# Performance work log

Hardware: AMD Instinct MI355X
Metric: run time of the kernel (lower is better)

## Reference

```python
import jax, jax.numpy as jnp
import numpy as np

D_MODEL = 1024
D_STATE = 16
D_CONV = 4
EXPAND = 2
D_INNER = EXPAND * D_MODEL  # 2048
BATCH = 2
SEQ = 2048


def setup_inputs() -> dict:
    key = jax.random.key(0)
    ks = jax.random.split(key, 7)
    s = 0.02
    x = jax.random.normal(ks[0], (BATCH, SEQ, D_MODEL), jnp.float32)
    in_proj_w = jax.random.normal(ks[1], (2 * D_INNER, D_MODEL), jnp.float32) * s
    conv_w = jax.random.normal(ks[2], (D_INNER, 1, D_CONV), jnp.float32) * s  # depthwise: groups=d_inner
    conv_b = jnp.zeros((D_INNER,), jnp.float32)
    x_proj_w = jax.random.normal(ks[3], (2 * D_STATE, D_INNER), jnp.float32) * s
    dt_proj_w = jax.random.normal(ks[4], (D_INNER, D_INNER), jnp.float32) * s
    dt_proj_b = jnp.zeros((D_INNER,), jnp.float32)
    # A = arange(1..d_state) repeated for each inner channel; A_log = log(A)
    A_log = jnp.log(jnp.tile(jnp.arange(1, D_STATE + 1, dtype=jnp.float32), (D_INNER, 1)))
    D_param = jnp.ones((D_INNER,), jnp.float32)
    out_proj_w = jax.random.normal(ks[5], (D_MODEL, D_INNER), jnp.float32) * s
    return {"x": x, "in_proj_w": in_proj_w, "conv_w": conv_w, "conv_b": conv_b,
            "x_proj_w": x_proj_w, "dt_proj_w": dt_proj_w, "dt_proj_b": dt_proj_b,
            "A_log": A_log, "D_param": D_param, "out_proj_w": out_proj_w}


def reference(x, in_proj_w, conv_w, conv_b, x_proj_w, dt_proj_w, dt_proj_b, A_log, D_param, out_proj_w):
    B, L, _ = x.shape
    # input projection -> [B, L, 2*d_inner], split into ssm path and gate
    xz = x @ in_proj_w.T
    x_ssm, z = jnp.split(xz, 2, axis=-1)

    # causal depthwise conv1d (torch pads both sides by d_conv-1 then slices [:L])
    xc = jnp.transpose(x_ssm, (0, 2, 1))  # [B, d_inner, L]
    xc = jnp.pad(xc, ((0, 0), (0, 0), (D_CONV - 1, 0)))
    xc = jax.lax.conv_general_dilated(
        xc, conv_w, window_strides=(1,), padding='VALID',
        dimension_numbers=('NCH', 'OIH', 'NCH'), feature_group_count=D_INNER)
    xc = xc + conv_b[None, :, None]
    x_act = jax.nn.silu(jnp.transpose(xc, (0, 2, 1)))  # [B, L, d_inner]

    delta = jax.nn.softplus(x_act @ dt_proj_w.T + dt_proj_b)  # [B, L, d_inner]
    bc = x_act @ x_proj_w.T                                   # [B, L, 2*d_state]
    B_p, C_p = jnp.split(bc, 2, axis=-1)

    A = -jnp.exp(A_log)  # [d_inner, d_state]

    def step(h, inp):
        u_i, d_i, B_i, C_i = inp  # [B,d], [B,d], [B,n], [B,n]
        dA = jnp.exp(d_i[..., None] * A)                       # [B, d, n]
        h = dA * h + (d_i * u_i)[..., None] * B_i[:, None, :]  # [B, d, n]
        y = jnp.einsum('bdn,bn->bd', h, C_i)
        return h, y

    h0 = jnp.zeros((B, D_INNER, D_STATE), x.dtype)
    seq = (jnp.swapaxes(x_act, 0, 1), jnp.swapaxes(delta, 0, 1),
           jnp.swapaxes(B_p, 0, 1), jnp.swapaxes(C_p, 0, 1))
    _, ys = jax.lax.scan(step, h0, seq)  # ys: [L, B, d_inner]
    y_ssm = jnp.swapaxes(ys, 0, 1) + x_act * D_param

    y = y_ssm * jax.nn.silu(z)
    return y @ out_proj_w.T
```

## Files before the change

kernel.cpp:

```cpp
#include <hip/hip_runtime.h>
#include <hip/hip_bf16.h>
#include <math.h>

#define DM 1024
#define DS 16
#define DI 2048
#define NB 2
#define LL 2048
#define BL (NB*LL)
#define LC 32
#define NC (LL/LC)

typedef __attribute__((ext_vector_type(8))) short short8;
typedef __attribute__((ext_vector_type(8))) unsigned short ushort8;
typedef __attribute__((ext_vector_type(4))) float f32x4;

__device__ __forceinline__ float silu_f(float x){ return x / (1.f + __expf(-x)); }
__device__ __forceinline__ float softplus_f(float x){ return (x > 15.f) ? x : log1pf(__expf(x)); }
__device__ __forceinline__ unsigned short f2bf(float f){
  unsigned u = __float_as_uint(f);
  u += 0x7fff + ((u >> 16) & 1);
  return (unsigned short)(u >> 16);
}
__device__ __forceinline__ float bf2f(unsigned short v){
  return __uint_as_float(((unsigned)v) << 16);
}

__global__ __launch_bounds__(256) void f2b_k(const float* __restrict__ src,
                                             unsigned short* __restrict__ dst, int n)
{
  int i = (blockIdx.x * 256 + threadIdx.x) * 8;
  if (i >= n) return;
  float4 v0 = *(const float4*)&src[i];
  float4 v1 = *(const float4*)&src[i + 4];
  ushort8 o;
  o[0]=f2bf(v0.x); o[1]=f2bf(v0.y); o[2]=f2bf(v0.z); o[3]=f2bf(v0.w);
  o[4]=f2bf(v1.x); o[5]=f2bf(v1.y); o[6]=f2bf(v1.z); o[7]=f2bf(v1.w);
  *(ushort8*)&dst[i] = o;
}

__global__ __launch_bounds__(256) void f2b_multi(
    const float* __restrict__ s0, unsigned short* __restrict__ d0, int c0,
    const float* __restrict__ s1, unsigned short* __restrict__ d1, int c1,
    const float* __restrict__ s2, unsigned short* __restrict__ d2, int c2,
    const float* __restrict__ s3, unsigned short* __restrict__ d3, int c3)
{
  int b = blockIdx.x;
  const float* s; unsigned short* d;
  if (b < c0)              { s = s0; d = d0; }
  else if ((b -= c0) < c1) { s = s1; d = d1; }
  else if ((b -= c1) < c2) { s = s2; d = d2; }
  else                     { b -= c2; s = s3; d = d3; }
  int i = (b * 256 + threadIdx.x) * 8;
  float4 v0 = *(const float4*)&s[i];
  float4 v1 = *(const float4*)&s[i + 4];
  ushort8 o;
  o[0]=f2bf(v0.x); o[1]=f2bf(v0.y); o[2]=f2bf(v0.z); o[3]=f2bf(v0.w);
  o[4]=f2bf(v1.x); o[5]=f2bf(v1.y); o[6]=f2bf(v1.z); o[7]=f2bf(v1.w);
  *(ushort8*)&d[i] = o;
}

template<int BN, int WAVESN, int EPI, int OUTBF>
__global__ __launch_bounds__(512, 2) void gemm3(
    const unsigned short* __restrict__ A, const unsigned short* __restrict__ Bw,
    const float* __restrict__ bias, void* __restrict__ Cp,
    int M, int N, int K)
{
  constexpr int BM = 256;
  constexpr int WM = BM / (8 / WAVESN);
  constexpr int WN = BN / WAVESN;
  constexpr int MR = WM / 16;
  constexpr int NRJ = WN / 16;
  constexpr int SLOADS = 4 + BN / 64;
  __shared__ unsigned short lds[2][(BM + BN) * 64];
  const int t = threadIdx.x;
  const int wid = t >> 6, lane = t & 63;
  const int nbx = N / BN;
  const int cpx = (nbx * (M / BM)) >> 3;
  const int bid = (int)blockIdx.x;
  const int swz = (bid & 7) * cpx + (bid >> 3);
  const int bm = (swz / nbx) * BM, bn = (swz % nbx) * BN;
  const int wm = (wid / WAVESN) * WM, wn = (wid % WAVESN) * WN;
  const int srow8 = lane >> 3;
  const int sch   = lane & 7;

  f32x4 acc[MR][NRJ] = {};

  auto stage = [&](int buf, int kt) {
    const int k0 = kt * 64;
    #pragma unroll
    for (int p = 0; p < 4; p++) {
      int row = p * 64 + wid * 8 + srow8;
      int ch = sch ^ (row & 7);
      __builtin_amdgcn_global_load_lds(
        (const __attribute__((address_space(1))) void*)(A + (size_t)(bm + row) * K + k0 + ch * 8),
        (__attribute__((address_space(3))) void*)(&lds[buf][(p * 64 + wid * 8) * 64]), 16, 0, 0);
    }
    #pragma unroll
    for (int p = 0; p < BN / 64; p++) {
      int row = p * 64 + wid * 8 + srow8;
      int ch = sch ^ (row & 7);
      __builtin_amdgcn_global_load_lds(
        (const __attribute__((address_space(1))) void*)(Bw + (size_t)(bn + row) * K + k0 + ch * 8),
        (__attribute__((address_space(3))) void*)(&lds[buf][(BM + p * 64 + wid * 8) * 64]), 16, 0, 0);
    }
  };

  const int nk = K / 64;
  stage(0, 0);
  stage(1, 1);
  asm volatile("s_waitcnt vmcnt(%0)" :: "n"(SLOADS) : "memory");
  __builtin_amdgcn_s_barrier();

  int cur = 0;
  for (int kt = 0; kt < nk; kt++) {
    const unsigned short* bufA = &lds[cur][0];
    const unsigned short* bufB = &lds[cur][BM * 64];
    #pragma unroll
    for (int ks = 0; ks < 2; ks++) {
      short8 af[MR], bfr[NRJ];
      #pragma unroll
      for (int i = 0; i < MR; i++) {
        int r = wm + i * 16 + (lane & 15);
        int c = ((ks << 2) + (lane >> 4)) ^ (r & 7);
        af[i] = *(const short8*)&bufA[r * 64 + c * 8];
      }
      #pragma unroll
      for (int j = 0; j < NRJ; j++) {
        int r = wn + j * 16 + (lane & 15);
        int c = ((ks << 2) + (lane >> 4)) ^ (r & 7);
        bfr[j] = *(const short8*)&bufB[r * 64 + c * 8];
      }
      #pragma unroll
      for (int i = 0; i < MR; i++)
        #pragma unroll
        for (int j = 0; j < NRJ; j++)
          acc[i][j] = __builtin_amdgcn_mfma_f32_16x16x32_bf16(af[i], bfr[j], acc[i][j], 0, 0, 0);
    }
    if (kt < nk - 2) {
      __builtin_amdgcn_s_barrier();
      stage(cur, kt + 2);
      asm volatile("s_waitcnt vmcnt(%0)" :: "n"(SLOADS) : "memory");
      __builtin_amdgcn_s_barrier();
    } else if (kt == nk - 2) {
      asm volatile("s_waitcnt vmcnt(0)" ::: "memory");
      __builtin_amdgcn_s_barrier();
    }
    cur ^= 1;
  }

  #pragma unroll
  for (int i = 0; i < MR; i++) {
    #pragma unroll
    for (int j = 0; j < NRJ; j++) {
      int col = bn + wn + j * 16 + (lane & 15);
      float bv = (EPI == 1) ? bias[col] : 0.f;
      #pragma unroll
      for (int r = 0; r < 4; r++) {
        int row = bm + wm + i * 16 + (lane >> 4) * 4 + r;
        float v = acc[i][j][r];
        if (EPI == 1) v = softplus_f(v + bv);
        if (OUTBF) ((unsigned short*)Cp)[(size_t)row * N + col] = f2bf(v);
        else       ((float*)Cp)[(size_t)row * N + col] = v;
      }
    }
  }
}

__global__ __launch_bounds__(256) void conv_silu_k(
    const unsigned short* __restrict__ xz, const float* __restrict__ cw,
    const float* __restrict__ cb, unsigned short* __restrict__ xa)
{
  int v = blockIdx.x * 256 + threadIdx.x;
  int d8 = (v & (DI/8 - 1)) * 8;
  int bl = v >> 8;
  int l  = bl & (LL - 1);
  float acc[8];
  #pragma unroll
  for (int j = 0; j < 8; j++) acc[j] = cb[d8 + j];
  size_t rowb = (size_t)bl * (2 * DI) + d8;
  #pragma unroll
  for (int k = 0; k < 4; k++) {
    int ls = l - 3 + k;
    if (ls >= 0) {
      ushort8 xv = *(const ushort8*)&xz[rowb + (size_t)(k - 3) * (2 * DI)];
      #pragma unroll
      for (int j = 0; j < 8; j++) acc[j] += bf2f(xv[j]) * cw[(d8 + j) * 4 + k];
    }
  }
  ushort8 o;
  #pragma unroll
  for (int j = 0; j < 8; j++) o[j] = f2bf(silu_f(acc[j]));
  *(ushort8*)&xa[(size_t)bl * DI + d8] = o;
}

__global__ __launch_bounds__(256) void bc_k(
    const unsigned short* __restrict__ xa, const unsigned short* __restrict__ w,
    float* __restrict__ bc)
{
  __shared__ unsigned short sx[8 * DI];
  const int t = threadIdx.x;
  const size_t base = (size_t)blockIdx.x * 8 * DI;
  #pragma unroll
  for (int it = 0; it < 8; it++) {
    int v = t + it * 256;
    *(ushort8*)&sx[v * 8] = *(const ushort8*)&xa[base + (size_t)v * 8];
  }
  __syncthreads();
  const int m = t >> 5, n = t & 31;
  const unsigned short* wr = w + (size_t)n * DI;
  const unsigned short* xr = sx + m * DI;
  float acc = 0.f;
  #pragma unroll 4
  for (int k = 0; k < DI; k += 8) {
    ushort8 xv = *(const ushort8*)&xr[k];
    ushort8 wv = *(const ushort8*)&wr[k];
    #pragma unroll
    for (int j = 0; j < 8; j++) acc += bf2f(xv[j]) * bf2f(wv[j]);
  }
  bc[(size_t)(blockIdx.x * 8 + m) * 32 + n] = acc;
}

__global__ __launch_bounds__(256) void scan_part1(
    const float* __restrict__ dlt, const unsigned short* __restrict__ xa,
    const float* __restrict__ bc, const float* __restrict__ A_log,
    float* __restrict__ S_arr, float* __restrict__ sumdlt)
{
  const int bid = blockIdx.x;
  const int b = bid >> 9;
  const int c = (bid >> 3) & (NC - 1);
  const int dg = bid & 7;
  const int t = threadIdx.x;
  const int d = dg * 256 + t;
  float Ac[16];
  #pragma unroll
  for (int n = 0; n < 16; n++) Ac[n] = -__expf(A_log[d * 16 + n]);
  __shared__ float sB[LC][16];
  for (int e = t; e < LC * 16; e += 256) {
    int l = e >> 4, n = e & 15;
    sB[l][n] = bc[(size_t)(b * LL + c * LC + l) * 32 + n];
  }
  __syncthreads();
  float h[16] = {};
  float sd = 0.f;
  size_t rowbase = (size_t)(b * LL + c * LC) * DI + d;
  for (int l = 0; l < LC; l++) {
    float dl = dlt[rowbase + (size_t)l * DI];
    float u  = bf2f(xa[rowbase + (size_t)l * DI]);
    float w = dl * u;
    sd += dl;
    #pragma unroll
    for (int n = 0; n < 16; n++) {
      float dA = __expf(dl * Ac[n]);
      h[n] = dA * h[n] + w * sB[l][n];
    }
  }
  float* Sp = S_arr + ((size_t)(b * NC + c) * DI + d) * 16;
  #pragma unroll
  for (int n = 0; n < 16; n++) Sp[n] = h[n];
  sumdlt[(size_t)(b * NC + c) * DI + d] = sd;
}

__global__ __launch_bounds__(256) void scan_combine(
    const float* __restrict__ A_log, const float* __restrict__ sumdlt,
    float* __restrict__ S_arr)
{
  int tid = blockIdx.x * 256 + threadIdx.x;
  int n = tid & 15;
  int d = (tid >> 4) & (DI - 1);
  int b = tid >> 15;
  float Ac = -__expf(A_log[d * 16 + n]);
  float h = 0.f;
  for (int c = 0; c < NC; c++) {
    size_t idx = ((size_t)(b * NC + c) * DI + d) * 16 + n;
    float S = S_arr[idx];
    float P = __expf(sumdlt[(size_t)(b * NC + c) * DI + d] * Ac);
    S_arr[idx] = h;
    h = P * h + S;
  }
}

__global__ __launch_bounds__(256) void scan_part2(
    const float* __restrict__ dlt, const unsigned short* __restrict__ xa,
    const float* __restrict__ bc, const float* __restrict__ A_log,
    const float* __restrict__ Dp, const unsigned short* __restrict__ xz,
    const float* __restrict__ Hin, unsigned short* __restrict__ y)
{
  const int bid = blockIdx.x;
  const int b = bid >> 9;
  const int c = (bid >> 3) & (NC - 1);
  const int dg = bid & 7;
  const int t = threadIdx.x;
  const int d = dg * 256 + t;
  float Ac[16];
  #pragma unroll
  for (int n = 0; n < 16; n++) Ac[n] = -__expf(A_log[d * 16 + n]);
  __shared__ float sB[LC][16];
  __shared__ float sC[LC][16];
  for (int e = t; e < LC * 16; e += 256) {
    int l = e >> 4, n = e & 15;
    size_t row = (size_t)(b * LL + c * LC + l) * 32;
    sB[l][n] = bc[row + n];
    sC[l][n] = bc[row + 16 + n];
  }
  __syncthreads();
  float h[16];
  const float* Hp = Hin + ((size_t)(b * NC + c) * DI + d) * 16;
  #pragma unroll
  for (int n = 0; n < 16; n++) h[n] = Hp[n];
  const float Dv = Dp[d];
  size_t rowbase = (size_t)(b * LL + c * LC) * DI + d;
  for (int l = 0; l < LC; l++) {
    float dl = dlt[rowbase + (size_t)l * DI];
    float u  = bf2f(xa[rowbase + (size_t)l * DI]);
    float w = dl * u;
    float ya = 0.f;
    #pragma unroll
    for (int n = 0; n < 16; n++) {
      float dA = __expf(dl * Ac[n]);
      h[n] = dA * h[n] + w * sB[l][n];
      ya += h[n] * sC[l][n];
    }
    float zz = bf2f(xz[(size_t)(b * LL + c * LC + l) * (2 * DI) + DI + d]);
    y[rowbase + (size_t)l * DI] = f2bf((ya + u * Dv) * silu_f(zz));
  }
}

extern "C" void kernel_launch(void* const* d_in, const int* in_sizes, int n_in,
                              void* d_out, int out_size, void* d_ws, size_t ws_size,
                              hipStream_t stream)
{
  const float* x    = (const float*)d_in[0];
  const float* Win  = (const float*)d_in[1];
  const float* cw   = (const float*)d_in[2];
  const float* cb   = (const float*)d_in[3];
  const float* Wxp  = (const float*)d_in[4];
  const float* Wdt  = (const float*)d_in[5];
  const float* bdt  = (const float*)d_in[6];
  const float* Alog = (const float*)d_in[7];
  const float* Dp   = (const float*)d_in[8];
  const float* Wout = (const float*)d_in[9];
  float* out = (float*)d_out;

  float* ws = (float*)d_ws;
  float* dlt    = ws;
  float* bcb    = dlt + 8388608;
  float* S_arr  = bcb + 131072;
  float* sumdlt = S_arr + 4194304;
  unsigned short* xz_bf = (unsigned short*)(sumdlt + 262144);
  unsigned short* xa_bf = xz_bf + 16777216;
  unsigned short* y_bf  = xa_bf + 8388608;
  unsigned short* x_bf  = y_bf;
  unsigned short* win_bf= y_bf + 4194304;
  unsigned short* wbuf  = y_bf + 8388608;
  unsigned short* wxp_bf= wbuf + 4194304;

  f2b_multi<<<dim3(2048 + 2048 + 2048 + 32), dim3(256), 0, stream>>>(
      x, x_bf, 2048, Win, win_bf, 2048, Wdt, wbuf, 2048, Wxp, wxp_bf, 32);
  gemm3<256,4,0,1><<<dim3(256), dim3(512), 0, stream>>>(x_bf, win_bf, nullptr, xz_bf, BL, 2*DI, DM);
  conv_silu_k<<<dim3(BL*DI/8/256), dim3(256), 0, stream>>>(xz_bf, cw, cb, xa_bf);
  gemm3<128,2,1,0><<<dim3(256), dim3(512), 0, stream>>>(xa_bf, wbuf, bdt, dlt, BL, DI, DI);
  f2b_k<<<dim3(DM*DI/2048), dim3(256), 0, stream>>>(Wout, wbuf, DM*DI);
  bc_k<<<dim3(BL/8), dim3(256), 0, stream>>>(xa_bf, wxp_bf, bcb);
  scan_part1<<<dim3(NB*NC*8), dim3(256), 0, stream>>>(dlt, xa_bf, bcb, Alog, S_arr, sumdlt);
  scan_combine<<<dim3(NB*DI*DS/256), dim3(256), 0, stream>>>(Alog, sumdlt, S_arr);
  scan_part2<<<dim3(NB*NC*8), dim3(256), 0, stream>>>(dlt, xa_bf, bcb, Alog, Dp, xz_bf, S_arr, y_bf);
  gemm3<64,2,0,0><<<dim3(256), dim3(512), 0, stream>>>(y_bf, wbuf, nullptr, out, BL, DM, DI);
}
```

Measured before the change: 346.5 us.

## Replace GEMM with triple-buffered, compile-time-K pipeline and retune tile shapes

Replaces the double-buffered GEMM with a triple-buffered version that prefetches three K-tiles ahead and fully unrolls the K loop using a compile-time K. Tile shapes change: all GEMMs use a 4x2 wave layout, and the in-projection uses 256x128 tiles over 512 blocks. The swizzle in the LDS fragment reads is simplified to lane-based XOR, which matches the store swizzle because row&7 equals lane&7 for these rows. Launch bounds drop to one block per CU, trading occupancy for deeper prefetch and more LDS.

```diff
diff --git a/kernel.cpp b/kernel.cpp
--- a/kernel.cpp
+++ b/kernel.cpp
@@ -60,27 +60,27 @@
   *(ushort8*)&d[i] = o;
 }
 
-template<int BN, int WAVESN, int EPI, int OUTBF>
-__global__ __launch_bounds__(512, 2) void gemm3(
+template<int BM, int BN, int KK, int EPI, int OUTBF>
+__global__ __launch_bounds__(512, 1) void gemm4(
     const unsigned short* __restrict__ A, const unsigned short* __restrict__ Bw,
     const float* __restrict__ bias, void* __restrict__ Cp,
-    int M, int N, int K)
-{
-  constexpr int BM = 256;
-  constexpr int WM = BM / (8 / WAVESN);
-  constexpr int WN = BN / WAVESN;
+    int M, int N)
+{
+  constexpr int WM = BM / 4;
+  constexpr int WN = BN / 2;
   constexpr int MR = WM / 16;
   constexpr int NRJ = WN / 16;
-  constexpr int SLOADS = 4 + BN / 64;
-  __shared__ unsigned short lds[2][(BM + BN) * 64];
+  constexpr int SL = (BM + BN) / 64;
+  constexpr int NK = KK / 64;
+  __shared__ unsigned short lds[3][(BM + BN) * 64];
   const int t = threadIdx.x;
   const int wid = t >> 6, lane = t & 63;
   const int nbx = N / BN;
-  const int cpx = (nbx * (M / BM)) >> 3;
+  const int cpx = (int)gridDim.x >> 3;
   const int bid = (int)blockIdx.x;
   const int swz = (bid & 7) * cpx + (bid >> 3);
   const int bm = (swz / nbx) * BM, bn = (swz % nbx) * BN;
-  const int wm = (wid / WAVESN) * WM, wn = (wid % WAVESN) * WN;
+  const int wm = (wid >> 1) * WM, wn = (wid & 1) * WN;
   const int srow8 = lane >> 3;
   const int sch   = lane & 7;
 
@@ -89,11 +89,11 @@
   auto stage = [&](int buf, int kt) {
     const int k0 = kt * 64;
     #pragma unroll
-    for (int p = 0; p < 4; p++) {
+    for (int p = 0; p < BM / 64; p++) {
       int row = p * 64 + wid * 8 + srow8;
       int ch = sch ^ (row & 7);
       __builtin_amdgcn_global_load_lds(
-        (const __attribute__((address_space(1))) void*)(A + (size_t)(bm + row) * K + k0 + ch * 8),
+        (const __attribute__((address_space(1))) void*)(A + (size_t)(bm + row) * KK + k0 + ch * 8),
         (__attribute__((address_space(3))) void*)(&lds[buf][(p * 64 + wid * 8) * 64]), 16, 0, 0);
     }
     #pragma unroll
@@ -101,34 +101,27 @@
       int row = p * 64 + wid * 8 + srow8;
       int ch = sch ^ (row & 7);
       __builtin_amdgcn_global_load_lds(
-        (const __attribute__((address_space(1))) void*)(Bw + (size_t)(bn + row) * K + k0 + ch * 8),
+        (const __attribute__((address_space(1))) void*)(Bw + (size_t)(bn + row) * KK + k0 + ch * 8),
         (__attribute__((address_space(3))) void*)(&lds[buf][(BM + p * 64 + wid * 8) * 64]), 16, 0, 0);
     }
   };
 
-  const int nk = K / 64;
-  stage(0, 0);
-  stage(1, 1);
-  asm volatile("s_waitcnt vmcnt(%0)" :: "n"(SLOADS) : "memory");
-  __builtin_amdgcn_s_barrier();
-
-  int cur = 0;
-  for (int kt = 0; kt < nk; kt++) {
-    const unsigned short* bufA = &lds[cur][0];
-    const unsigned short* bufB = &lds[cur][BM * 64];
+  auto compute = [&](int buf) {
+    const unsigned short* bufA = &lds[buf][0];
+    const unsigned short* bufB = &lds[buf][BM * 64];
     #pragma unroll
     for (int ks = 0; ks < 2; ks++) {
       short8 af[MR], bfr[NRJ];
       #pragma unroll
       for (int i = 0; i < MR; i++) {
         int r = wm + i * 16 + (lane & 15);
-        int c = ((ks << 2) + (lane >> 4)) ^ (r & 7);
+        int c = ((ks << 2) + (lane >> 4)) ^ (lane & 7);
         af[i] = *(const short8*)&bufA[r * 64 + c * 8];
       }
       #pragma unroll
       for (int j = 0; j < NRJ; j++) {
         int r = wn + j * 16 + (lane & 15);
-        int c = ((ks << 2) + (lane >> 4)) ^ (r & 7);
+        int c = ((ks << 2) + (lane >> 4)) ^ (lane & 7);
         bfr[j] = *(const short8*)&bufB[r * 64 + c * 8];
       }
       #pragma unroll
@@ -137,17 +130,27 @@
         for (int j = 0; j < NRJ; j++)
           acc[i][j] = __builtin_amdgcn_mfma_f32_16x16x32_bf16(af[i], bfr[j], acc[i][j], 0, 0, 0);
     }
-    if (kt < nk - 2) {
-      __builtin_amdgcn_s_barrier();
-      stage(cur, kt + 2);
-      asm volatile("s_waitcnt vmcnt(%0)" :: "n"(SLOADS) : "memory");
-      __builtin_amdgcn_s_barrier();
-    } else if (kt == nk - 2) {
-      asm volatile("s_waitcnt vmcnt(0)" ::: "memory");
-      __builtin_amdgcn_s_barrier();
-    }
-    cur ^= 1;
-  }
+  };
+
+  stage(0, 0); stage(1, 1); stage(2, 2);
+  asm volatile("s_waitcnt vmcnt(%0)" :: "n"(2 * SL) : "memory");
+  __builtin_amdgcn_s_barrier();
+
+  #pragma unroll
+  for (int kt = 0; kt <= NK - 4; kt++) {
+    compute(kt % 3);
+    __builtin_amdgcn_s_barrier();
+    stage(kt % 3, kt + 3);
+    asm volatile("s_waitcnt vmcnt(%0)" :: "n"(2 * SL) : "memory");
+    __builtin_amdgcn_s_barrier();
+  }
+  compute((NK - 3) % 3);
+  asm volatile("s_waitcnt vmcnt(%0)" :: "n"(SL) : "memory");
+  __builtin_amdgcn_s_barrier();
+  compute((NK - 2) % 3);
+  asm volatile("s_waitcnt vmcnt(0)" ::: "memory");
+  __builtin_amdgcn_s_barrier();
+  compute((NK - 1) % 3);
 
   #pragma unroll
   for (int i = 0; i < MR; i++) {
@@ -357,13 +360,13 @@
 
   f2b_multi<<<dim3(2048 + 2048 + 2048 + 32), dim3(256), 0, stream>>>(
       x, x_bf, 2048, Win, win_bf, 2048, Wdt, wbuf, 2048, Wxp, wxp_bf, 32);
-  gemm3<256,4,0,1><<<dim3(256), dim3(512), 0, stream>>>(x_bf, win_bf, nullptr, xz_bf, BL, 2*DI, DM);
+  gemm4<256,128,1024,0,1><<<dim3(512), dim3(512), 0, stream>>>(x_bf, win_bf, nullptr, xz_bf, BL, 2*DI);
   conv_silu_k<<<dim3(BL*DI/8/256), dim3(256), 0, stream>>>(xz_bf, cw, cb, xa_bf);
-  gemm3<128,2,1,0><<<dim3(256), dim3(512), 0, stream>>>(xa_bf, wbuf, bdt, dlt, BL, DI, DI);
+  gemm4<256,128,2048,1,0><<<dim3(256), dim3(512), 0, stream>>>(xa_bf, wbuf, bdt, dlt, BL, DI);
   f2b_k<<<dim3(DM*DI/2048), dim3(256), 0, stream>>>(Wout, wbuf, DM*DI);
   bc_k<<<dim3(BL/8), dim3(256), 0, stream>>>(xa_bf, wxp_bf, bcb);
   scan_part1<<<dim3(NB*NC*8), dim3(256), 0, stream>>>(dlt, xa_bf, bcb, Alog, S_arr, sumdlt);
   scan_combine<<<dim3(NB*DI*DS/256), dim3(256), 0, stream>>>(Alog, sumdlt, S_arr);
   scan_part2<<<dim3(NB*NC*8), dim3(256), 0, stream>>>(dlt, xa_bf, bcb, Alog, Dp, xz_bf, S_arr, y_bf);
-  gemm3<64,2,0,0><<<dim3(256), dim3(512), 0, stream>>>(y_bf, wbuf, nullptr, out, BL, DM, DI);
-}
+  gemm4<256,64,2048,0,0><<<dim3(256), dim3(512), 0, stream>>>(y_bf, wbuf, nullptr, out, BL, DM);
+}
```

After: 337.1 us. 1.03x faster.

## Replace templated GEMM with fixed 128x256 tile and overlapped load/MFMA schedule

Applied to the files above, without the earlier changes.

Replaces the gemm3 template, which used a 256-row tile and per-GEMM N widths, with gemm5, which uses a fixed 128x256 tile, 8 waves of 64x64, and launch bounds of one block per SIMD set. The main loop now reads all LDS fragments first, issues the next global->LDS stage, and then runs the MFMAs behind sched_barriers, so memory traffic overlaps compute. All three GEMMs use the new kernel with adjusted grid sizes. The output GEMM drops to 128 blocks, which risks underfilling the GPU, and the larger register footprint lowers occupancy.

```diff
diff --git a/kernel.cpp b/kernel.cpp
--- a/kernel.cpp
+++ b/kernel.cpp
@@ -60,99 +60,102 @@
   *(ushort8*)&d[i] = o;
 }
 
-template<int BN, int WAVESN, int EPI, int OUTBF>
-__global__ __launch_bounds__(512, 2) void gemm3(
+template<int EPI, int OUTBF>
+__global__ __launch_bounds__(512, 1) void gemm5(
     const unsigned short* __restrict__ A, const unsigned short* __restrict__ Bw,
     const float* __restrict__ bias, void* __restrict__ Cp,
-    int M, int N, int K)
-{
-  constexpr int BM = 256;
-  constexpr int WM = BM / (8 / WAVESN);
-  constexpr int WN = BN / WAVESN;
-  constexpr int MR = WM / 16;
-  constexpr int NRJ = WN / 16;
-  constexpr int SLOADS = 4 + BN / 64;
+    int N, int K)
+{
+  constexpr int BM = 128, BN = 256;
   __shared__ unsigned short lds[2][(BM + BN) * 64];
-  const int t = threadIdx.x;
-  const int wid = t >> 6, lane = t & 63;
+  const int t0 = threadIdx.x;
+  const int wid = t0 >> 6, lane = t0 & 63;
   const int nbx = N / BN;
-  const int cpx = (nbx * (M / BM)) >> 3;
+  const int cpx = (int)gridDim.x >> 3;
   const int bid = (int)blockIdx.x;
   const int swz = (bid & 7) * cpx + (bid >> 3);
   const int bm = (swz / nbx) * BM, bn = (swz % nbx) * BN;
-  const int wm = (wid / WAVESN) * WM, wn = (wid % WAVESN) * WN;
-  const int srow8 = lane >> 3;
-  const int sch   = lane & 7;
-
-  f32x4 acc[MR][NRJ] = {};
+  const int wm = (wid >> 2) * 64, wn = (wid & 3) * 64;
+
+  f32x4 acc[4][4] = {};
 
   auto stage = [&](int buf, int kt) {
     const int k0 = kt * 64;
     #pragma unroll
-    for (int p = 0; p < 4; p++) {
-      int row = p * 64 + wid * 8 + srow8;
-      int ch = sch ^ (row & 7);
+    for (int s = 0; s < 6; s++) {
+      int g = wid * 6 + s;
+      int row = g * 8 + (lane >> 3);
+      int ch  = (lane & 7) ^ (lane >> 3);
+      const unsigned short* src;
+      if (g < 16) src = A  + (size_t)(bm + row) * K + k0 + ch * 8;
+      else        src = Bw + (size_t)(bn + row - BM) * K + k0 + ch * 8;
       __builtin_amdgcn_global_load_lds(
-        (const __attribute__((address_space(1))) void*)(A + (size_t)(bm + row) * K + k0 + ch * 8),
-        (__attribute__((address_space(3))) void*)(&lds[buf][(p * 64 + wid * 8) * 64]), 16, 0, 0);
-    }
-    #pragma unroll
-    for (int p = 0; p < BN / 64; p++) {
-      int row = p * 64 + wid * 8 + srow8;
-      int ch = sch ^ (row & 7);
-      __builtin_amdgcn_global_load_lds(
-        (const __attribute__((address_space(1))) void*)(Bw + (size_t)(bn + row) * K + k0 + ch * 8),
-        (__attribute__((address_space(3))) void*)(&lds[buf][(BM + p * 64 + wid * 8) * 64]), 16, 0, 0);
+          (const __attribute__((address_space(1))) void*)src,
+          (__attribute__((address_space(3))) void*)(&lds[buf][(size_t)g * 512]), 16, 0, 0);
     }
   };
 
-  const int nk = K / 64;
   stage(0, 0);
   stage(1, 1);
-  asm volatile("s_waitcnt vmcnt(%0)" :: "n"(SLOADS) : "memory");
+  asm volatile("s_waitcnt vmcnt(6)" ::: "memory");
   __builtin_amdgcn_s_barrier();
 
-  int cur = 0;
-  for (int kt = 0; kt < nk; kt++) {
-    const unsigned short* bufA = &lds[cur][0];
-    const unsigned short* bufB = &lds[cur][BM * 64];
-    #pragma unroll
-    for (int ks = 0; ks < 2; ks++) {
-      short8 af[MR], bfr[NRJ];
-      #pragma unroll
-      for (int i = 0; i < MR; i++) {
-        int r = wm + i * 16 + (lane & 15);
-        int c = ((ks << 2) + (lane >> 4)) ^ (r & 7);
-        af[i] = *(const short8*)&bufA[r * 64 + c * 8];
-      }
-      #pragma unroll
-      for (int j = 0; j < NRJ; j++) {
-        int r = wn + j * 16 + (lane & 15);
-        int c = ((ks << 2) + (lane >> 4)) ^ (r & 7);
-        bfr[j] = *(const short8*)&bufB[r * 64 + c * 8];
-      }
-      #pragma unroll
-      for (int i = 0; i < MR; i++)
-        #pragma unroll
-        for (int j = 0; j < NRJ; j++)
-          acc[i][j] = __builtin_amdgcn_mfma_f32_16x16x32_bf16(af[i], bfr[j], acc[i][j], 0, 0, 0);
-    }
-    if (kt < nk - 2) {
-      __builtin_amdgcn_s_barrier();
-      stage(cur, kt + 2);
-      asm volatile("s_waitcnt vmcnt(%0)" :: "n"(SLOADS) : "memory");
-      __builtin_amdgcn_s_barrier();
-    } else if (kt == nk - 2) {
-      asm volatile("s_waitcnt vmcnt(0)" ::: "memory");
-      __builtin_amdgcn_s_barrier();
-    }
-    cur ^= 1;
-  }
-
-  #pragma unroll
-  for (int i = 0; i < MR; i++) {
-    #pragma unroll
-    for (int j = 0; j < NRJ; j++) {
+  const int nk = K >> 6;
+
+#define G5_READS(Q)                                                          \
+  short8 af[2][4], bfr[2][4];                                                \
+  _Pragma("unroll")                                                          \
+  for (int ks = 0; ks < 2; ks++) {                                           \
+    int cc = ((ks << 2) + (lane >> 4)) ^ (lane & 7);                         \
+    _Pragma("unroll")                                                        \
+    for (int i = 0; i < 4; i++) {                                            \
+      af[ks][i]  = *(const short8*)&lds[Q][(wm + i * 16 + (lane & 15)) * 64 + cc * 8]; \
+      bfr[ks][i] = *(const short8*)&lds[Q][BM * 64 + (wn + i * 16 + (lane & 15)) * 64 + cc * 8]; \
+    }                                                                        \
+  }
+
+#define G5_MFMA()                                                            \
+  _Pragma("unroll")                                                          \
+  for (int ks = 0; ks < 2; ks++)                                             \
+    _Pragma("unroll")                                                        \
+    for (int i = 0; i < 4; i++)                                              \
+      _Pragma("unroll")                                                      \
+      for (int j = 0; j < 4; j++)                                            \
+        acc[i][j] = __builtin_amdgcn_mfma_f32_16x16x32_bf16(af[ks][i], bfr[ks][j], acc[i][j], 0, 0, 0);
+
+  for (int t = 0; t < nk - 2; t++) {
+    const int q = t & 1;
+    G5_READS(q)
+    asm volatile("s_waitcnt lgkmcnt(0)" ::: "memory");
+    __builtin_amdgcn_sched_barrier(0);
+    __builtin_amdgcn_s_barrier();
+    stage(q, t + 2);
+    __builtin_amdgcn_sched_barrier(0);
+    G5_MFMA()
+    __builtin_amdgcn_sched_barrier(0);
+    asm volatile("s_waitcnt vmcnt(6)" ::: "memory");
+    __builtin_amdgcn_s_barrier();
+  }
+  {
+    const int q = (nk - 2) & 1;
+    G5_READS(q)
+    G5_MFMA()
+    __builtin_amdgcn_sched_barrier(0);
+    asm volatile("s_waitcnt vmcnt(0)" ::: "memory");
+    __builtin_amdgcn_s_barrier();
+  }
+  {
+    const int q = (nk - 1) & 1;
+    G5_READS(q)
+    G5_MFMA()
+  }
+#undef G5_READS
+#undef G5_MFMA
+
+  #pragma unroll
+  for (int i = 0; i < 4; i++) {
+    #pragma unroll
+    for (int j = 0; j < 4; j++) {
       int col = bn + wn + j * 16 + (lane & 15);
       float bv = (EPI == 1) ? bias[col] : 0.f;
       #pragma unroll
@@ -357,13 +360,13 @@
 
   f2b_multi<<<dim3(2048 + 2048 + 2048 + 32), dim3(256), 0, stream>>>(
       x, x_bf, 2048, Win, win_bf, 2048, Wdt, wbuf, 2048, Wxp, wxp_bf, 32);
-  gemm3<256,4,0,1><<<dim3(256), dim3(512), 0, stream>>>(x_bf, win_bf, nullptr, xz_bf, BL, 2*DI, DM);
+  gemm5<0,1><<<dim3(512), dim3(512), 0, stream>>>(x_bf, win_bf, nullptr, xz_bf, 2*DI, DM);
   conv_silu_k<<<dim3(BL*DI/8/256), dim3(256), 0, stream>>>(xz_bf, cw, cb, xa_bf);
-  gemm3<128,2,1,0><<<dim3(256), dim3(512), 0, stream>>>(xa_bf, wbuf, bdt, dlt, BL, DI, DI);
+  gemm5<1,0><<<dim3(256), dim3(512), 0, stream>>>(xa_bf, wbuf, bdt, dlt, DI, DI);
   f2b_k<<<dim3(DM*DI/2048), dim3(256), 0, stream>>>(Wout, wbuf, DM*DI);
   bc_k<<<dim3(BL/8), dim3(256), 0, stream>>>(xa_bf, wxp_bf, bcb);
   scan_part1<<<dim3(NB*NC*8), dim3(256), 0, stream>>>(dlt, xa_bf, bcb, Alog, S_arr, sumdlt);
   scan_combine<<<dim3(NB*DI*DS/256), dim3(256), 0, stream>>>(Alog, sumdlt, S_arr);
   scan_part2<<<dim3(NB*NC*8), dim3(256), 0, stream>>>(dlt, xa_bf, bcb, Alog, Dp, xz_bf, S_arr, y_bf);
-  gemm3<64,2,0,0><<<dim3(256), dim3(512), 0, stream>>>(y_bf, wbuf, nullptr, out, BL, DM, DI);
-}
+  gemm5<0,0><<<dim3(128), dim3(512), 0, stream>>>(y_bf, wbuf, nullptr, out, DM, DI);
+}
```

Result: slower. 363.2 us (+4.8%).
